# Optimization experiments

Measured on AMD Instinct MI355X. Metric: run time of the kernel, lower is better.

Reference implementation:

```python
import jax, jax.numpy as jnp
import numpy as np

OH, OW, SCALE = 14, 14, 1.0
N, C, H, W = 1, 256, 200, 200
K = 1024


def setup_inputs() -> dict:
    key = jax.random.key(0)
    k1, k2, k3 = jax.random.split(key, 3)
    data = jax.random.normal(k1, (N, C, H, W), dtype=jnp.float32)
    # boxes: xmin,ymin,xmax,ymax with min<max, in-range
    xpair = jnp.sort(jax.random.uniform(k2, (K, 2), minval=0.0, maxval=float(W)), axis=1)
    ypair = jnp.sort(jax.random.uniform(k3, (K, 2), minval=0.0, maxval=float(H)), axis=1)
    boxes = jnp.stack([xpair[:, 0], ypair[:, 0], xpair[:, 1], ypair[:, 1]], axis=1)
    return {"data": data, "boxes": boxes}


def crop_resize(data, boxes):
    boxes = boxes / SCALE
    img = data[0].reshape(C, H * W)  # flattened spatial for gather
    xs = jnp.arange(OW, dtype=jnp.float32)
    ys = jnp.arange(OH, dtype=jnp.float32)
    a11 = (boxes[:, 2] - boxes[:, 0]) / OW  # [K]
    a22 = (boxes[:, 3] - boxes[:, 1]) / OH
    xi = a11[:, None] * xs[None, :] + boxes[:, 0:1]  # [K,OW] pixel x coords
    yi = a22[:, None] * ys[None, :] + boxes[:, 1:2]  # [K,OH]
    # normalize to [-1,1] as in the torch module
    gx = (xi - W / 2) / W * 2
    gy = (yi - H / 2) / H * 2
    # grid_sample (align_corners=False, zeros padding): unnormalize
    ux = ((gx + 1.0) * W - 1.0) / 2.0  # [K,OW]
    uy = ((gy + 1.0) * H - 1.0) / 2.0  # [K,OH]
    x = jnp.broadcast_to(ux[:, None, :], (K, OH, OW))
    y = jnp.broadcast_to(uy[:, :, None], (K, OH, OW))
    x0 = jnp.floor(x)
    y0 = jnp.floor(y)
    wx1 = x - x0
    wy1 = y - y0
    x0i = x0.astype(jnp.int32)
    y0i = y0.astype(jnp.int32)

    def gather(yc, xc):
        valid = (yc >= 0) & (yc < H) & (xc >= 0) & (xc < W)
        flat = jnp.clip(yc, 0, H - 1) * W + jnp.clip(xc, 0, W - 1)
        v = jnp.take(img, flat.reshape(-1), axis=1).reshape(C, K, OH, OW)
        return v * valid.astype(img.dtype)[None]

    out = (gather(y0i, x0i) * ((1 - wy1) * (1 - wx1))[None]
           + gather(y0i, x0i + 1) * ((1 - wy1) * wx1)[None]
           + gather(y0i + 1, x0i) * (wy1 * (1 - wx1))[None]
           + gather(y0i + 1, x0i + 1) * (wy1 * wx1)[None])
    return jnp.transpose(out, (1, 0, 2, 3))  # [K,C,OH,OW]


def reference(data, boxes):
    return crop_resize(data, boxes)
```

## Files before the change

kernel.cpp:

```cpp
#include <hip/hip_runtime.h>
#include <hip/hip_bf16.h>

#define CC   256
#define HH   200
#define WW   200
#define KK   1024
#define OH_  14
#define OW_  14
#define OHW  196
#define HW   (HH * WW)
#define NG   8
#define GCH  32
#define ROWB (GCH * 2)
#define PA   100
#define PB   96

static __device__ __forceinline__ float lo_bf(unsigned int u) {
  union { unsigned int i; float f; } x; x.i = u << 16; return x.f;
}
static __device__ __forceinline__ float hi_bf(unsigned int u) {
  union { unsigned int i; float f; } x; x.i = u & 0xFFFF0000u; return x.f;
}

__global__ __launch_bounds__(256) void transpose_bf16_kernel(
    const float* __restrict__ img, unsigned short* __restrict__ ws) {
  __shared__ float tile[64][66];
  const int hw0 = blockIdx.x * 64;
  const int c0  = blockIdx.y * 64;
#pragma unroll
  for (int j = 0; j < 4; ++j) {
    const int idx = j * 256 + threadIdx.x;
    const int c   = idx >> 4;
    const int x   = (idx & 15) * 4;
    const float4 v = *(const float4*)&img[(size_t)(c0 + c) * HW + hw0 + x];
    *(float2*)&tile[c][x]     = make_float2(v.x, v.y);
    *(float2*)&tile[c][x + 2] = make_float2(v.z, v.w);
  }
  __syncthreads();
#pragma unroll
  for (int j = 0; j < 4; ++j) {
    const int l   = j * 256 + threadIdx.x;
    const int gg  = l >> 9;
    const int rem = l & 511;
    const int r   = rem >> 3;
    const int q   = rem & 7;
    const int cl  = gg * 32 + 4 * q;
    const float a = tile[cl + 0][r];
    const float b = tile[cl + 1][r];
    const float c = tile[cl + 2][r];
    const float d = tile[cl + 3][r];
    const __hip_bfloat16 ba = __float2bfloat16(a);
    const __hip_bfloat16 bb = __float2bfloat16(b);
    const __hip_bfloat16 bc = __float2bfloat16(c);
    const __hip_bfloat16 bd = __float2bfloat16(d);
    const unsigned int lo = (unsigned int)*(const unsigned short*)&ba |
                            ((unsigned int)*(const unsigned short*)&bb << 16);
    const unsigned int hi = (unsigned int)*(const unsigned short*)&bc |
                            ((unsigned int)*(const unsigned short*)&bd << 16);
    const int G = (c0 >> 5) + gg;
    *(uint2*)&ws[(size_t)G * HW * GCH + (size_t)(hw0 + r) * GCH + 4 * q] =
        make_uint2(lo, hi);
  }
}

__device__ __forceinline__ void precompute_pos(
    const float* __restrict__ boxes, int k, int tid,
    int4* sidx, float4* sw, int idx_scale) {
  if (tid < OHW) {
    const float xmin = boxes[k * 4 + 0];
    const float ymin = boxes[k * 4 + 1];
    const float xmax = boxes[k * 4 + 2];
    const float ymax = boxes[k * 4 + 3];
    const float a11 = (xmax - xmin) / 14.0f;
    const float a22 = (ymax - ymin) / 14.0f;
    const int ow = tid % OW_;
    const int oh = tid / OW_;
    const float xi = a11 * (float)ow + xmin;
    const float yi = a22 * (float)oh + ymin;
    const float gx = (xi - 100.0f) / 200.0f * 2.0f;
    const float gy = (yi - 100.0f) / 200.0f * 2.0f;
    const float x  = ((gx + 1.0f) * 200.0f - 1.0f) * 0.5f;
    const float y  = ((gy + 1.0f) * 200.0f - 1.0f) * 0.5f;
    const float fx0 = floorf(x);
    const float fy0 = floorf(y);
    const float wx = x - fx0;
    const float wy = y - fy0;
    const int x0 = (int)fx0, y0 = (int)fy0;
    const int x1 = x0 + 1,   y1 = y0 + 1;
    const bool vx0 = (x0 >= 0) & (x0 < WW);
    const bool vx1 = (x1 >= 0) & (x1 < WW);
    const bool vy0 = (y0 >= 0) & (y0 < HH);
    const bool vy1 = (y1 >= 0) & (y1 < HH);
    const int cx0 = min(max(x0, 0), WW - 1);
    const int cx1 = min(max(x1, 0), WW - 1);
    const int cy0 = min(max(y0, 0), HH - 1);
    const int cy1 = min(max(y1, 0), HH - 1);
    sidx[tid] = make_int4((cy0 * WW + cx0) * idx_scale, (cy0 * WW + cx1) * idx_scale,
                          (cy1 * WW + cx0) * idx_scale, (cy1 * WW + cx1) * idx_scale);
    sw[tid] = make_float4((1.0f - wy) * (1.0f - wx) * (float)(vy0 && vx0),
                          (1.0f - wy) * wx          * (float)(vy0 && vx1),
                          wy          * (1.0f - wx) * (float)(vy1 && vx0),
                          wy          * wx          * (float)(vy1 && vx1));
  }
}

#define GATHER_ONE(pos_, p_)                                                  \
  {                                                                           \
    const int4   id = sidx[p_];                                               \
    const float4 wt = sw[p_];                                                 \
    const unsigned int u0 = *(const unsigned int*)(wsb + id.x);               \
    const unsigned int u1 = *(const unsigned int*)(wsb + id.y);               \
    const unsigned int u2 = *(const unsigned int*)(wsb + id.z);               \
    const unsigned int u3 = *(const unsigned int*)(wsb + id.w);               \
    tile[pos_][2 * cp]     = wt.x * lo_bf(u0) + wt.y * lo_bf(u1) +            \
                             wt.z * lo_bf(u2) + wt.w * lo_bf(u3);             \
    tile[pos_][2 * cp + 1] = wt.x * hi_bf(u0) + wt.y * hi_bf(u1) +            \
                             wt.z * hi_bf(u2) + wt.w * hi_bf(u3);             \
  }

__global__ __launch_bounds__(256, 8) void crop_resize_bf16(
    const unsigned short* __restrict__ ws, const float* __restrict__ boxes,
    float* __restrict__ out) {
  __shared__ int4   sidx[OHW];
  __shared__ float4 sw[OHW];
  __shared__ float  tile[PA][33];

  const int b   = blockIdx.x;
  const int g   = b & 7;
  const int k   = b >> 3;
  const int tid = threadIdx.x;
  precompute_pos(boxes, k, tid, sidx, sw, ROWB);
  __syncthreads();

  const int cp = tid & 15;
  const int po = tid >> 4;
  const char* wsb = (const char*)ws + ((size_t)g * HW * GCH * 2 + cp * 4);
  char* ob = (char*)out + (((size_t)k * CC + g * GCH) * OHW) * 4;

#pragma unroll 3
  for (int it = 0; it < 6; ++it) {
    const int pos = po + it * 16;
    GATHER_ONE(pos, pos);
  }
  if (po < 4) {
    const int pos = 96 + po;
    GATHER_ONE(pos, pos);
  }
  __syncthreads();
  for (int j = tid; j < GCH * 25; j += 256) {
    const int cc = j / 25;
    const int pp = j - cc * 25;
    const float4 v = make_float4(tile[4 * pp][cc],     tile[4 * pp + 1][cc],
                                 tile[4 * pp + 2][cc], tile[4 * pp + 3][cc]);
    *(float4*)(ob + (size_t)cc * (OHW * 4) + pp * 16) = v;
  }
  __syncthreads();

#pragma unroll 3
  for (int it = 0; it < 6; ++it) {
    const int pos = 100 + po + it * 16;
    GATHER_ONE(pos - 100, pos);
  }
  __syncthreads();
  for (int j = tid; j < GCH * 24; j += 256) {
    const int cc = j / 24;
    const int pp = j - cc * 24;
    const float4 v = make_float4(tile[4 * pp][cc],     tile[4 * pp + 1][cc],
                                 tile[4 * pp + 2][cc], tile[4 * pp + 3][cc]);
    *(float4*)(ob + (size_t)cc * (OHW * 4) + 400 + pp * 16) = v;
  }
}

#define NCHUNK 32
#define CPB    (CC / NCHUNK)
__global__ __launch_bounds__(256) void crop_resize_direct(
    const float* __restrict__ img, const float* __restrict__ boxes,
    float* __restrict__ out) {
  __shared__ int4   sidx[OHW];
  __shared__ float4 sw[OHW];
  const int k      = blockIdx.x;
  const int cchunk = blockIdx.y;
  const int tid    = threadIdx.x;
  precompute_pos(boxes, k, tid, sidx, sw, 1);
  __syncthreads();

  const int c0 = cchunk * CPB;
  const int total = CPB * OHW;
  float* outk = out + (size_t)k * CC * OHW + (size_t)c0 * OHW;
  const float* imgc0 = img + (size_t)c0 * HW;

#pragma unroll 4
  for (int i = tid; i < total; i += 256) {
    const int c   = i / OHW;
    const int pos = i - c * OHW;
    const int4   id = sidx[pos];
    const float4 wd = sw[pos];
    const float* p  = imgc0 + c * HW;
    const float v = wd.x * p[id.x] + wd.y * p[id.y] +
                    wd.z * p[id.z] + wd.w * p[id.w];
    outk[i] = v;
  }
}

extern "C" void kernel_launch(void* const* d_in, const int* in_sizes, int n_in,
                              void* d_out, int out_size, void* d_ws, size_t ws_size,
                              hipStream_t stream) {
  const float* img   = (const float*)d_in[0];
  const float* boxes = (const float*)d_in[1];
  float* out = (float*)d_out;
  const size_t need = (size_t)HW * CC * sizeof(unsigned short);
  if (ws_size >= need) {
    unsigned short* wsimg = (unsigned short*)d_ws;
    hipLaunchKernelGGL(transpose_bf16_kernel, dim3(HW / 64, CC / 64), dim3(256),
                       0, stream, img, wsimg);
    hipLaunchKernelGGL(crop_resize_bf16, dim3(KK * NG), dim3(256), 0, stream,
                       wsimg, boxes, out);
  } else {
    hipLaunchKernelGGL(crop_resize_direct, dim3(KK, NCHUNK), dim3(256), 0,
                       stream, img, boxes, out);
  }
}
```

Baseline: 63.91 us.

## Software-pipeline bf16 gathers across three store phases with register prefetch

Restructures the gather kernel into three 64-position phases. Each phase's gather loads are issued into registers before the previous phase's tile is written back, so global-memory latency overlaps with the shared-memory transpose and output stores. The shared tile shrinks to 68 rows, and launch bounds drop from 8 to 6 blocks per SM to leave room for the extra live registers. The costs are lower occupancy and one more barrier pair.

```diff
diff --git a/kernel.cpp b/kernel.cpp
--- a/kernel.cpp
+++ b/kernel.cpp
@@ -12,8 +12,6 @@
 #define NG   8
 #define GCH  32
 #define ROWB (GCH * 2)
-#define PA   100
-#define PB   96
 
 static __device__ __forceinline__ float lo_bf(unsigned int u) {
   union { unsigned int i; float f; } x; x.i = u << 16; return x.f;
@@ -104,26 +102,12 @@
   }
 }
 
-#define GATHER_ONE(pos_, p_)                                                  \
-  {                                                                           \
-    const int4   id = sidx[p_];                                               \
-    const float4 wt = sw[p_];                                                 \
-    const unsigned int u0 = *(const unsigned int*)(wsb + id.x);               \
-    const unsigned int u1 = *(const unsigned int*)(wsb + id.y);               \
-    const unsigned int u2 = *(const unsigned int*)(wsb + id.z);               \
-    const unsigned int u3 = *(const unsigned int*)(wsb + id.w);               \
-    tile[pos_][2 * cp]     = wt.x * lo_bf(u0) + wt.y * lo_bf(u1) +            \
-                             wt.z * lo_bf(u2) + wt.w * lo_bf(u3);             \
-    tile[pos_][2 * cp + 1] = wt.x * hi_bf(u0) + wt.y * hi_bf(u1) +            \
-                             wt.z * hi_bf(u2) + wt.w * hi_bf(u3);             \
-  }
-
-__global__ __launch_bounds__(256, 8) void crop_resize_bf16(
+__global__ __launch_bounds__(256, 6) void crop_resize_bf16(
     const unsigned short* __restrict__ ws, const float* __restrict__ boxes,
     float* __restrict__ out) {
   __shared__ int4   sidx[OHW];
   __shared__ float4 sw[OHW];
-  __shared__ float  tile[PA][33];
+  __shared__ float  tile[68][33];
 
   const int b   = blockIdx.x;
   const int g   = b & 7;
@@ -137,38 +121,66 @@
   const char* wsb = (const char*)ws + ((size_t)g * HW * GCH * 2 + cp * 4);
   char* ob = (char*)out + (((size_t)k * CC + g * GCH) * OHW) * 4;
 
-#pragma unroll 3
-  for (int it = 0; it < 6; ++it) {
-    const int pos = po + it * 16;
-    GATHER_ONE(pos, pos);
-  }
-  if (po < 4) {
-    const int pos = 96 + po;
-    GATHER_ONE(pos, pos);
-  }
-  __syncthreads();
-  for (int j = tid; j < GCH * 25; j += 256) {
-    const int cc = j / 25;
-    const int pp = j - cc * 25;
-    const float4 v = make_float4(tile[4 * pp][cc],     tile[4 * pp + 1][cc],
-                                 tile[4 * pp + 2][cc], tile[4 * pp + 3][cc]);
-    *(float4*)(ob + (size_t)cc * (OHW * 4) + pp * 16) = v;
-  }
-  __syncthreads();
-
-#pragma unroll 3
-  for (int it = 0; it < 6; ++it) {
-    const int pos = 100 + po + it * 16;
-    GATHER_ONE(pos - 100, pos);
-  }
-  __syncthreads();
-  for (int j = tid; j < GCH * 24; j += 256) {
-    const int cc = j / 24;
-    const int pp = j - cc * 24;
-    const float4 v = make_float4(tile[4 * pp][cc],     tile[4 * pp + 1][cc],
-                                 tile[4 * pp + 2][cc], tile[4 * pp + 3][cc]);
-    *(float4*)(ob + (size_t)cc * (OHW * 4) + 400 + pp * 16) = v;
-  }
+  unsigned int u[5][4];
+
+#define ISSUE4(slot_, p_)                                                     \
+  {                                                                           \
+    const int4 id = sidx[p_];                                                 \
+    u[slot_][0] = *(const unsigned int*)(wsb + id.x);                         \
+    u[slot_][1] = *(const unsigned int*)(wsb + id.y);                         \
+    u[slot_][2] = *(const unsigned int*)(wsb + id.z);                         \
+    u[slot_][3] = *(const unsigned int*)(wsb + id.w);                         \
+  }
+#define CONSUME(slot_, p_, row_)                                              \
+  {                                                                           \
+    const float4 wt = sw[p_];                                                 \
+    tile[row_][2 * cp]     = wt.x * lo_bf(u[slot_][0]) +                      \
+                             wt.y * lo_bf(u[slot_][1]) +                      \
+                             wt.z * lo_bf(u[slot_][2]) +                      \
+                             wt.w * lo_bf(u[slot_][3]);                       \
+    tile[row_][2 * cp + 1] = wt.x * hi_bf(u[slot_][0]) +                      \
+                             wt.y * hi_bf(u[slot_][1]) +                      \
+                             wt.z * hi_bf(u[slot_][2]) +                      \
+                             wt.w * hi_bf(u[slot_][3]);                       \
+  }
+#define STORE(cb_, nf4_)                                                      \
+  for (int j = tid; j < GCH * (nf4_); j += 256) {                             \
+    const int cc = j / (nf4_);                                                \
+    const int q  = j - cc * (nf4_);                                           \
+    const float4 v = make_float4(tile[4 * q][cc],     tile[4 * q + 1][cc],    \
+                                 tile[4 * q + 2][cc], tile[4 * q + 3][cc]);   \
+    *(float4*)(ob + (size_t)cc * (OHW * 4) + (cb_) * 4 + q * 16) = v;         \
+  }
+
+#pragma unroll
+  for (int i = 0; i < 4; ++i) ISSUE4(i, po + 16 * i);
+
+#pragma unroll
+  for (int i = 0; i < 4; ++i) CONSUME(i, po + 16 * i, po + 16 * i);
+#pragma unroll
+  for (int i = 0; i < 4; ++i) ISSUE4(i, 64 + po + 16 * i);
+  __syncthreads();
+  STORE(0, 16)
+  __syncthreads();
+
+#pragma unroll
+  for (int i = 0; i < 4; ++i) CONSUME(i, 64 + po + 16 * i, po + 16 * i);
+#pragma unroll
+  for (int i = 0; i < 4; ++i) ISSUE4(i, 128 + po + 16 * i);
+  if (po < 4) ISSUE4(4, 192 + po);
+  __syncthreads();
+  STORE(64, 16)
+  __syncthreads();
+
+#pragma unroll
+  for (int i = 0; i < 4; ++i) CONSUME(i, 128 + po + 16 * i, po + 16 * i);
+  if (po < 4) CONSUME(4, 192 + po, 64 + po);
+  __syncthreads();
+  STORE(128, 17)
+
+#undef ISSUE4
+#undef CONSUME
+#undef STORE
 }
 
 #define NCHUNK 32
```

Result: no change. 63.96 us (+0.1%).

## Write gathered bf16 results directly to global as float4, dropping LDS transpose tile

Applied to the files above, without the earlier changes.

Each thread now computes four consecutive output positions for its channel pair and stores them straight to global memory as 16-byte vector writes, instead of staging 100-position tiles in shared memory and transposing them. This removes the LDS tile, two passes and several __syncthreads barriers. In exchange, store coalescing changes: the 16 lanes sharing a position group write to different channel rows that are 784 bytes apart, so a wavefront's stores are scattered rather than contiguous. Work per thread also becomes less even, since only 16 threads handle the last quad.

```diff
diff --git a/kernel.cpp b/kernel.cpp
--- a/kernel.cpp
+++ b/kernel.cpp
@@ -12,8 +12,8 @@
 #define NG   8
 #define GCH  32
 #define ROWB (GCH * 2)
-#define PA   100
-#define PB   96
+
+typedef float f32x4 __attribute__((ext_vector_type(4)));
 
 static __device__ __forceinline__ float lo_bf(unsigned int u) {
   union { unsigned int i; float f; } x; x.i = u << 16; return x.f;
@@ -104,7 +104,7 @@
   }
 }
 
-#define GATHER_ONE(pos_, p_)                                                  \
+#define POS_ONE(p_, vlo_, vhi_)                                               \
   {                                                                           \
     const int4   id = sidx[p_];                                               \
     const float4 wt = sw[p_];                                                 \
@@ -112,10 +112,21 @@
     const unsigned int u1 = *(const unsigned int*)(wsb + id.y);               \
     const unsigned int u2 = *(const unsigned int*)(wsb + id.z);               \
     const unsigned int u3 = *(const unsigned int*)(wsb + id.w);               \
-    tile[pos_][2 * cp]     = wt.x * lo_bf(u0) + wt.y * lo_bf(u1) +            \
-                             wt.z * lo_bf(u2) + wt.w * lo_bf(u3);             \
-    tile[pos_][2 * cp + 1] = wt.x * hi_bf(u0) + wt.y * hi_bf(u1) +            \
-                             wt.z * hi_bf(u2) + wt.w * hi_bf(u3);             \
+    vlo_ = wt.x * lo_bf(u0) + wt.y * lo_bf(u1) +                              \
+           wt.z * lo_bf(u2) + wt.w * lo_bf(u3);                               \
+    vhi_ = wt.x * hi_bf(u0) + wt.y * hi_bf(u1) +                              \
+           wt.z * hi_bf(u2) + wt.w * hi_bf(u3);                               \
+  }
+
+#define QUAD(Q_)                                                              \
+  {                                                                           \
+    float l0, l1, l2, l3, h0, h1, h2, h3;                                     \
+    POS_ONE(4 * (Q_) + 0, l0, h0);                                            \
+    POS_ONE(4 * (Q_) + 1, l1, h1);                                            \
+    POS_ONE(4 * (Q_) + 2, l2, h2);                                            \
+    POS_ONE(4 * (Q_) + 3, l3, h3);                                            \
+    *(f32x4*)(ob + 16 * (Q_))            = (f32x4){l0, l1, l2, l3};           \
+    *(f32x4*)(ob + OHW * 4 + 16 * (Q_))  = (f32x4){h0, h1, h2, h3};           \
   }
 
 __global__ __launch_bounds__(256, 8) void crop_resize_bf16(
@@ -123,7 +134,6 @@
     float* __restrict__ out) {
   __shared__ int4   sidx[OHW];
   __shared__ float4 sw[OHW];
-  __shared__ float  tile[PA][33];
 
   const int b   = blockIdx.x;
   const int g   = b & 7;
@@ -133,42 +143,15 @@
   __syncthreads();
 
   const int cp = tid & 15;
-  const int po = tid >> 4;
+  const int qb = tid >> 4;
   const char* wsb = (const char*)ws + ((size_t)g * HW * GCH * 2 + cp * 4);
-  char* ob = (char*)out + (((size_t)k * CC + g * GCH) * OHW) * 4;
-
-#pragma unroll 3
-  for (int it = 0; it < 6; ++it) {
-    const int pos = po + it * 16;
-    GATHER_ONE(pos, pos);
-  }
-  if (po < 4) {
-    const int pos = 96 + po;
-    GATHER_ONE(pos, pos);
-  }
-  __syncthreads();
-  for (int j = tid; j < GCH * 25; j += 256) {
-    const int cc = j / 25;
-    const int pp = j - cc * 25;
-    const float4 v = make_float4(tile[4 * pp][cc],     tile[4 * pp + 1][cc],
-                                 tile[4 * pp + 2][cc], tile[4 * pp + 3][cc]);
-    *(float4*)(ob + (size_t)cc * (OHW * 4) + pp * 16) = v;
-  }
-  __syncthreads();
-
-#pragma unroll 3
-  for (int it = 0; it < 6; ++it) {
-    const int pos = 100 + po + it * 16;
-    GATHER_ONE(pos - 100, pos);
-  }
-  __syncthreads();
-  for (int j = tid; j < GCH * 24; j += 256) {
-    const int cc = j / 24;
-    const int pp = j - cc * 24;
-    const float4 v = make_float4(tile[4 * pp][cc],     tile[4 * pp + 1][cc],
-                                 tile[4 * pp + 2][cc], tile[4 * pp + 3][cc]);
-    *(float4*)(ob + (size_t)cc * (OHW * 4) + 400 + pp * 16) = v;
-  }
+  char* ob = (char*)out +
+             (((size_t)k * CC + g * GCH + 2 * cp) * OHW) * 4;
+
+  QUAD(qb)
+  QUAD(qb + 16)
+  QUAD(qb + 32)
+  if (tid < 16) QUAD(48)
 }
 
 #define NCHUNK 32
```

After: 76.90 us. 1.2x slower.
